# Optimization experiments

Measured on AMD Instinct MI355X. Metric: run time of the kernel, lower is better.

## Reference

```python
import jax, jax.numpy as jnp
import numpy as np

ALPHA_F, ALPHA_L, ALPHA_E, V_E = 0.1, 1.0, 1.0, 10.0
DF = float(np.exp(-ALPHA_F))
DL = float(np.exp(-ALPHA_L))
DE = float(np.exp(-ALPHA_E))

B, T, C, H, W = 8, 10, 32, 128, 128


def _fixed_weight(chans, dtype):
    # [[0.5,1,0.5],[1,0,1],[0.5,1,0.5]] broadcast to [C, C, 3, 3]
    k = jnp.array([[0.5, 1.0, 0.5], [1.0, 0.0, 1.0], [0.5, 1.0, 0.5]], dtype=dtype)
    return jnp.broadcast_to(k, (chans, chans, 3, 3))


def _conv(y, w):
    # 3x3 same-padding conv, NCHW / OIHW
    return jax.lax.conv_general_dilated(
        y, w, window_strides=(1, 1), padding='SAME',
        dimension_numbers=('NCHW', 'OIHW', 'NCHW'))


def setup_inputs() -> dict:
    key = jax.random.key(0)
    k1, k2, k3 = jax.random.split(key, 3)
    x = jax.random.normal(k1, (B, T, C, H, W), dtype=jnp.float32)
    # small-scale conv weights (fan-in-ish) to keep sigmoid in its dynamic range
    conv_w = jax.random.normal(k2, (C, C, 3, 3), dtype=jnp.float32) * 0.05
    conv_b = jax.random.normal(k3, (C,), dtype=jnp.float32) * 0.05
    return {'x': x, 'conv_w': conv_w, 'conv_b': conv_b}


def reference(x, conv_w, conv_b):
    b, t, c, h, w = x.shape
    wf = _fixed_weight(c, x.dtype)  # fixed, non-trainable feedback kernel
    bias = conv_b[None, :, None, None]

    def step(carry, x_t):
        f, l, e, y = carry
        f = DF * f + _conv(y, conv_w) + bias + x_t
        l = DL * l + _conv(y, wf)
        u = f + 0.5 * f * l
        e = DE * e + V_E * y
        y = jax.nn.sigmoid(u - e)
        return (f, l, e, y), y

    z = jnp.zeros((b, c, h, w), x.dtype)
    e0 = jnp.full((b, c, h, w), V_E / ALPHA_E, x.dtype)
    xs = jnp.moveaxis(x, 1, 0)  # [T, B, C, H, W]
    _, ys = jax.lax.scan(step, (z, z, e0, z), xs)
    return jnp.moveaxis(ys, 0, 1)  # [B, T, C, H, W]
```

## Files before the change

### kernel.cpp

```cpp
#include <hip/hip_runtime.h>
#include <math.h>

namespace {

constexpr int B = 8, T = 10, C = 32, H = 128, W = 128;
constexpr int HW = H * W;
constexpr int CHW = C * HW;
constexpr int BHW = B * HW;
constexpr long long NSTATE = (long long)B * CHW;

constexpr float DF = 0.90483741803595952f;
constexpr float DL = 0.36787944117144233f;
constexpr float DE = 0.36787944117144233f;
constexpr float VE = 10.0f;
constexpr float E0 = 3.6787944117144233f;

__global__ void k_wtr(const float* __restrict__ wgt, float* __restrict__ wtr) {
  int i = blockIdx.x * 256 + threadIdx.x;
  if (i >= C * C * 9) return;
  int ci = i / 288;
  int k = (i / 32) % 9;
  int co = i & 31;
  wtr[i] = wgt[co * 288 + ci * 9 + k];
}

__launch_bounds__(256, 2)
__global__ void k_step0(const float* __restrict__ x, const float* __restrict__ bias,
                        float* __restrict__ f, float* __restrict__ e,
                        float* __restrict__ lpl, float* __restrict__ out,
                        float* __restrict__ s_out) {
  __shared__ float sred[8][32][4];
  const int tid = threadIdx.x, bid = blockIdx.x;
  const int tw = bid & 7, th = (bid >> 3) & 15, b = bid >> 7;
  const int h0 = th * 8, w0 = tw * 16;
  const int g = tid >> 5, s = tid & 31;
  const int sh = s >> 2, sw = s & 3, cb = 4 * sw;
  const int gh = h0 + sh, gwc = w0 + cb;
  const float4 bc4 = *(const float4*)&bias[4 * g];
  const float bc[4] = {bc4.x, bc4.y, bc4.z, bc4.w};

  float sp[4] = {0.f, 0.f, 0.f, 0.f};
#pragma unroll
  for (int q = 0; q < 4; ++q) {
    const int c = 4 * g + q;
    const size_t sidx = (size_t)b * CHW + (size_t)c * HW + (size_t)gh * W + gwc;
    const size_t oidx = (((size_t)b * T) * C + c) * (size_t)HW + (size_t)gh * W + gwc;
    float4 x4 = *(const float4*)(x + oidx);
    float xr[4] = {x4.x, x4.y, x4.z, x4.w};
    float fo[4], eo[4], yn[4];
#pragma unroll
    for (int p = 0; p < 4; ++p) {
      float fn = bc[q] + xr[p];
      float yy = 1.f / (1.f + __expf(E0 - fn));
      fo[p] = fn;
      eo[p] = DE * E0 + VE * yy;
      yn[p] = yy;
      sp[p] += yy;
    }
    *(float4*)(f + sidx) = make_float4(fo[0], fo[1], fo[2], fo[3]);
    *(float4*)(e + sidx) = make_float4(eo[0], eo[1], eo[2], eo[3]);
    *(float4*)(out + oidx) = make_float4(yn[0], yn[1], yn[2], yn[3]);
  }
  *(float4*)&sred[g][s][0] = make_float4(sp[0], sp[1], sp[2], sp[3]);
  __syncthreads();
  if (tid < 32) {
    float4 a = *(const float4*)&sred[0][tid][0];
#pragma unroll
    for (int gg = 1; gg < 8; ++gg) {
      float4 bq = *(const float4*)&sred[gg][tid][0];
      a.x += bq.x; a.y += bq.y; a.z += bq.z; a.w += bq.w;
    }
    const size_t pidx = (size_t)b * HW + (size_t)gh * W + gwc;
    *(float4*)(s_out + pidx) = a;
    *(float4*)(lpl + pidx) = make_float4(0.f, 0.f, 0.f, 0.f);
  }
}

__launch_bounds__(256, 2)
__global__ void k_step(const float* __restrict__ x, const float* __restrict__ wtr,
                       const float* __restrict__ bias, const float* __restrict__ s_in,
                       float* __restrict__ s_out, float* __restrict__ f,
                       float* __restrict__ e, float* __restrict__ lpl,
                       float* __restrict__ out, int t) {
  __shared__ float ysl[8][10][28];
  __shared__ float wsl[8][9][32];
  __shared__ float sl[10][21];
  __shared__ float sred[8][32][4];

  const int tid = threadIdx.x, bid = blockIdx.x;
  const int tw = bid & 7, th = (bid >> 3) & 15, b = bid >> 7;
  const int h0 = th * 8, w0 = tw * 16;
  const int g = tid >> 5, s = tid & 31;
  const int sh = s >> 2, sw = s & 3, cb = 4 * sw;
  const int gh = h0 + sh, gwc = w0 + cb;

  const float* ybase = out + ((size_t)b * T + (t - 1)) * CHW;

  for (int i = tid; i < 180; i += 256) {
    int rr = i / 18, cl = i % 18;
    int gh2 = h0 - 1 + rr, gw2 = w0 - 1 + cl;
    float v = 0.f;
    if ((unsigned)gh2 < (unsigned)H && (unsigned)gw2 < (unsigned)W)
      v = s_in[(size_t)b * HW + gh2 * W + gw2];
    sl[rr][cl] = v;
  }

  float4 l4 = *(const float4*)(lpl + (size_t)b * HW + (size_t)gh * W + gwc);
  float lnew[4] = {l4.x, l4.y, l4.z, l4.w};

  const int i0 = tid;
  const int cil0 = i0 / 60, rr0 = (i0 % 60) / 6, j0 = i0 % 6;
  const int gh0p = h0 - 1 + rr0, ws0p = w0 - 4 + 4 * j0;
  const bool ok0 = (unsigned)gh0p < (unsigned)H && (unsigned)ws0p <= (unsigned)(W - 4);
  const size_t yoff0 = (size_t)cil0 * HW + (size_t)(ok0 ? gh0p * W + ws0p : 0);
  float* const yd0 = &ysl[cil0][rr0][4 * j0];
  const int i1 = tid + 256;
  const bool use1 = i1 < 480;
  const int cil1 = (i1 / 60) & 7, rr1 = (i1 % 60) / 6, j1 = i1 % 6;
  const int gh1p = h0 - 1 + rr1, ws1p = w0 - 4 + 4 * j1;
  const bool ok1 = use1 && (unsigned)gh1p < (unsigned)H &&
                   (unsigned)ws1p <= (unsigned)(W - 4);
  const size_t yoff1 = (size_t)cil1 * HW + (size_t)(ok1 ? gh1p * W + ws1p : 0);
  float* const yd1 = &ysl[cil1][rr1][4 * j1];

  const float4* const wsrc = (const float4*)wtr;
  float4* const wlds = (float4*)&wsl[0][0][0];

  float4 y0v, y1v, w0v, w1v, w2v;
  auto prefetch = [&](int cc) {
    const float* yb = ybase + (size_t)cc * 8 * HW;
    y0v = ok0 ? *(const float4*)(yb + yoff0) : make_float4(0.f, 0.f, 0.f, 0.f);
    y1v = ok1 ? *(const float4*)(yb + yoff1) : make_float4(0.f, 0.f, 0.f, 0.f);
    const float4* wb = wsrc + cc * 576;
    w0v = wb[tid];
    w1v = wb[tid + 256];
    w2v = (tid < 64) ? wb[tid + 512] : make_float4(0.f, 0.f, 0.f, 0.f);
  };
  prefetch(0);

  float acc[4][4] = {};

#pragma unroll 1
  for (int cc = 0; cc < 4; ++cc) {
    __syncthreads();
    yd0[0] = y0v.x; yd0[1] = y0v.y; yd0[2] = y0v.z; yd0[3] = y0v.w;
    if (use1) { yd1[0] = y1v.x; yd1[1] = y1v.y; yd1[2] = y1v.z; yd1[3] = y1v.w; }
    wlds[tid] = w0v;
    wlds[tid + 256] = w1v;
    if (tid < 64) wlds[tid + 512] = w2v;
    __syncthreads();
    if (cc < 3) prefetch(cc + 1);
    if (cc == 0) {
      float linc[4];
#pragma unroll
      for (int p = 0; p < 4; ++p) {
        const int c0 = cb + p;
        linc[p] = 0.5f * (sl[sh][c0] + sl[sh][c0 + 2] + sl[sh + 2][c0] +
                          sl[sh + 2][c0 + 2]) +
                  sl[sh][c0 + 1] + sl[sh + 2][c0 + 1] + sl[sh + 1][c0] +
                  sl[sh + 1][c0 + 2];
      }
#pragma unroll
      for (int p = 0; p < 4; ++p) lnew[p] = DL * lnew[p] + linc[p];
    }
#pragma unroll
    for (int cil = 0; cil < 8; ++cil) {
#pragma unroll
      for (int kh = 0; kh < 3; ++kh) {
        const float* rowp = &ysl[cil][sh + kh][0];
        float2 a2 = *(const float2*)(rowp + cb + 2);
        float4 m4 = *(const float4*)(rowp + cb + 4);
        float2 z2 = *(const float2*)(rowp + cb + 8);
        const float yrow[6] = {a2.y, m4.x, m4.y, m4.z, m4.w, z2.x};
#pragma unroll
        for (int kw = 0; kw < 3; ++kw) {
          float4 wk = *(const float4*)&wsl[cil][3 * kh + kw][4 * g];
          const float wq[4] = {wk.x, wk.y, wk.z, wk.w};
#pragma unroll
          for (int q = 0; q < 4; ++q)
#pragma unroll
            for (int p = 0; p < 4; ++p)
              acc[q][p] = fmaf(wq[q], yrow[p + kw], acc[q][p]);
        }
      }
    }
  }

  const float4 bc4 = *(const float4*)&bias[4 * g];
  const float bc[4] = {bc4.x, bc4.y, bc4.z, bc4.w};
  float sp[4] = {0.f, 0.f, 0.f, 0.f};
#pragma unroll
  for (int q = 0; q < 4; ++q) {
    const int c = 4 * g + q;
    const size_t sidx = (size_t)b * CHW + (size_t)c * HW + (size_t)gh * W + gwc;
    const size_t oidx = (((size_t)b * T + t) * C + c) * (size_t)HW + (size_t)gh * W + gwc;
    float4 f4 = *(const float4*)(f + sidx);
    float4 e4 = *(const float4*)(e + sidx);
    float4 x4 = *(const float4*)(x + oidx);
    float fr[4] = {f4.x, f4.y, f4.z, f4.w};
    float er[4] = {e4.x, e4.y, e4.z, e4.w};
    float xr[4] = {x4.x, x4.y, x4.z, x4.w};
    float fo[4], eo[4], yn[4];
#pragma unroll
    for (int p = 0; p < 4; ++p) {
      float fn = DF * fr[p] + acc[q][p] + bc[q] + xr[p];
      float u = fmaf(0.5f * fn, lnew[p], fn);
      float yy = 1.f / (1.f + __expf(er[p] - u));
      fo[p] = fn;
      eo[p] = DE * er[p] + VE * yy;
      yn[p] = yy;
      sp[p] += yy;
    }
    *(float4*)(f + sidx) = make_float4(fo[0], fo[1], fo[2], fo[3]);
    *(float4*)(e + sidx) = make_float4(eo[0], eo[1], eo[2], eo[3]);
    *(float4*)(out + oidx) = make_float4(yn[0], yn[1], yn[2], yn[3]);
  }
  *(float4*)&sred[g][s][0] = make_float4(sp[0], sp[1], sp[2], sp[3]);
  __syncthreads();
  if (tid < 32) {
    float4 a = *(const float4*)&sred[0][tid][0];
#pragma unroll
    for (int gg = 1; gg < 8; ++gg) {
      float4 bq = *(const float4*)&sred[gg][tid][0];
      a.x += bq.x; a.y += bq.y; a.z += bq.z; a.w += bq.w;
    }
    const size_t pidx = (size_t)b * HW + (size_t)gh * W + gwc;
    *(float4*)(s_out + pidx) = a;
    *(float4*)(lpl + pidx) = make_float4(lnew[0], lnew[1], lnew[2], lnew[3]);
  }
}

}

extern "C" void kernel_launch(void* const* d_in, const int* in_sizes, int n_in,
                              void* d_out, int out_size, void* d_ws, size_t ws_size,
                              hipStream_t stream) {
  (void)in_sizes; (void)n_in; (void)out_size; (void)ws_size;
  const float* x = (const float*)d_in[0];
  const float* wgt = (const float*)d_in[1];
  const float* bias = (const float*)d_in[2];
  float* out = (float*)d_out;

  float* ws = (float*)d_ws;
  float* f = ws;
  float* e = f + NSTATE;
  float* lpl = e + NSTATE;
  float* sA = lpl + BHW;
  float* sB = sA + BHW;
  float* wtr = sB + BHW;

  k_wtr<<<36, 256, 0, stream>>>(wgt, wtr);
  k_step0<<<1024, 256, 0, stream>>>(x, bias, f, e, lpl, out, sA);

  float* s_in = sA;
  float* s_out = sB;
  for (int t = 1; t < T; ++t) {
    k_step<<<1024, 256, 0, stream>>>(x, wtr, bias, s_in, s_out, f, e, lpl, out, t);
    float* tmp = s_in; s_in = s_out; s_out = tmp;
  }
}
```

Baseline: 609.5 us.

## Split output channels across two blocks per tile to double grid parallelism

Each spatial tile is now handled by two blocks, each computing 16 of the 32 output channels, which doubles the grid to 2048 blocks. Each half writes its own partial channel-sum plane, and the next step adds the two planes when building the fixed-kernel feedback. Only half 0 updates the lateral state. The goal is better occupancy and latency hiding with fewer accumulators per thread. The cost is that every block still loads the full 32-channel input halo, so global and LDS traffic for y roughly doubles.

```diff
diff --git a/kernel.cpp b/kernel.cpp
--- a/kernel.cpp
+++ b/kernel.cpp
@@ -72,6 +72,7 @@
     }
     const size_t pidx = (size_t)b * HW + (size_t)gh * W + gwc;
     *(float4*)(s_out + pidx) = a;
+    *(float4*)(s_out + BHW + pidx) = make_float4(0.f, 0.f, 0.f, 0.f);
     *(float4*)(lpl + pidx) = make_float4(0.f, 0.f, 0.f, 0.f);
   }
 }
@@ -83,16 +84,18 @@
                        float* __restrict__ e, float* __restrict__ lpl,
                        float* __restrict__ out, int t) {
   __shared__ float ysl[8][10][28];
-  __shared__ float wsl[8][9][32];
+  __shared__ float wsl[8][9][16];
   __shared__ float sl[10][21];
   __shared__ float sred[8][32][4];
 
   const int tid = threadIdx.x, bid = blockIdx.x;
-  const int tw = bid & 7, th = (bid >> 3) & 15, b = bid >> 7;
+  const int half = bid & 1;
+  const int tw = (bid >> 1) & 7, th = (bid >> 4) & 15, b = bid >> 8;
   const int h0 = th * 8, w0 = tw * 16;
   const int g = tid >> 5, s = tid & 31;
   const int sh = s >> 2, sw = s & 3, cb = 4 * sw;
   const int gh = h0 + sh, gwc = w0 + cb;
+  const int cob = 16 * half;
 
   const float* ybase = out + ((size_t)b * T + (t - 1)) * CHW;
 
@@ -100,8 +103,10 @@
     int rr = i / 18, cl = i % 18;
     int gh2 = h0 - 1 + rr, gw2 = w0 - 1 + cl;
     float v = 0.f;
-    if ((unsigned)gh2 < (unsigned)H && (unsigned)gw2 < (unsigned)W)
-      v = s_in[(size_t)b * HW + gh2 * W + gw2];
+    if ((unsigned)gh2 < (unsigned)H && (unsigned)gw2 < (unsigned)W) {
+      const size_t ii = (size_t)b * HW + gh2 * W + gw2;
+      v = s_in[ii] + s_in[BHW + ii];
+    }
     sl[rr][cl] = v;
   }
 
@@ -125,29 +130,31 @@
 
   const float4* const wsrc = (const float4*)wtr;
   float4* const wlds = (float4*)&wsl[0][0][0];
-
-  float4 y0v, y1v, w0v, w1v, w2v;
+  const int wsl0 = tid;
+  const int wc0 = wsl0 / 36, wk0 = (wsl0 % 36) / 4, wj0 = wsl0 & 3;
+  const int wslot1 = tid + 256;
+  const bool wuse1 = wslot1 < 288;
+  const int wc1 = (wslot1 / 36) & 7, wk1 = (wslot1 % 36) / 4, wj1 = wslot1 & 3;
+
+  float4 y0v, y1v, w0v, w1v;
   auto prefetch = [&](int cc) {
     const float* yb = ybase + (size_t)cc * 8 * HW;
     y0v = ok0 ? *(const float4*)(yb + yoff0) : make_float4(0.f, 0.f, 0.f, 0.f);
     y1v = ok1 ? *(const float4*)(yb + yoff1) : make_float4(0.f, 0.f, 0.f, 0.f);
-    const float4* wb = wsrc + cc * 576;
-    w0v = wb[tid];
-    w1v = wb[tid + 256];
-    w2v = (tid < 64) ? wb[tid + 512] : make_float4(0.f, 0.f, 0.f, 0.f);
+    w0v = wsrc[((cc * 8 + wc0) * 9 + wk0) * 8 + 4 * half + wj0];
+    if (wuse1) w1v = wsrc[((cc * 8 + wc1) * 9 + wk1) * 8 + 4 * half + wj1];
   };
   prefetch(0);
 
-  float acc[4][4] = {};
+  float acc[2][4] = {};
 
 #pragma unroll 1
   for (int cc = 0; cc < 4; ++cc) {
     __syncthreads();
     yd0[0] = y0v.x; yd0[1] = y0v.y; yd0[2] = y0v.z; yd0[3] = y0v.w;
     if (use1) { yd1[0] = y1v.x; yd1[1] = y1v.y; yd1[2] = y1v.z; yd1[3] = y1v.w; }
-    wlds[tid] = w0v;
-    wlds[tid + 256] = w1v;
-    if (tid < 64) wlds[tid + 512] = w2v;
+    wlds[wsl0] = w0v;
+    if (wuse1) wlds[wslot1] = w1v;
     __syncthreads();
     if (cc < 3) prefetch(cc + 1);
     if (cc == 0) {
@@ -174,10 +181,10 @@
         const float yrow[6] = {a2.y, m4.x, m4.y, m4.z, m4.w, z2.x};
 #pragma unroll
         for (int kw = 0; kw < 3; ++kw) {
-          float4 wk = *(const float4*)&wsl[cil][3 * kh + kw][4 * g];
-          const float wq[4] = {wk.x, wk.y, wk.z, wk.w};
-#pragma unroll
-          for (int q = 0; q < 4; ++q)
+          float2 wk = *(const float2*)&wsl[cil][3 * kh + kw][2 * g];
+          const float wq[2] = {wk.x, wk.y};
+#pragma unroll
+          for (int q = 0; q < 2; ++q)
 #pragma unroll
             for (int p = 0; p < 4; ++p)
               acc[q][p] = fmaf(wq[q], yrow[p + kw], acc[q][p]);
@@ -186,12 +193,12 @@
     }
   }
 
-  const float4 bc4 = *(const float4*)&bias[4 * g];
-  const float bc[4] = {bc4.x, bc4.y, bc4.z, bc4.w};
+  const float2 bc2 = *(const float2*)&bias[cob + 2 * g];
+  const float bc[2] = {bc2.x, bc2.y};
   float sp[4] = {0.f, 0.f, 0.f, 0.f};
 #pragma unroll
-  for (int q = 0; q < 4; ++q) {
-    const int c = 4 * g + q;
+  for (int q = 0; q < 2; ++q) {
+    const int c = cob + 2 * g + q;
     const size_t sidx = (size_t)b * CHW + (size_t)c * HW + (size_t)gh * W + gwc;
     const size_t oidx = (((size_t)b * T + t) * C + c) * (size_t)HW + (size_t)gh * W + gwc;
     float4 f4 = *(const float4*)(f + sidx);
@@ -225,8 +232,9 @@
       a.x += bq.x; a.y += bq.y; a.z += bq.z; a.w += bq.w;
     }
     const size_t pidx = (size_t)b * HW + (size_t)gh * W + gwc;
-    *(float4*)(s_out + pidx) = a;
-    *(float4*)(lpl + pidx) = make_float4(lnew[0], lnew[1], lnew[2], lnew[3]);
+    *(float4*)(s_out + (size_t)half * BHW + pidx) = a;
+    if (half == 0)
+      *(float4*)(lpl + pidx) = make_float4(lnew[0], lnew[1], lnew[2], lnew[3]);
   }
 }
 
@@ -246,8 +254,8 @@
   float* e = f + NSTATE;
   float* lpl = e + NSTATE;
   float* sA = lpl + BHW;
-  float* sB = sA + BHW;
-  float* wtr = sB + BHW;
+  float* sB = sA + 2 * BHW;
+  float* wtr = sB + 2 * BHW;
 
   k_wtr<<<36, 256, 0, stream>>>(wgt, wtr);
   k_step0<<<1024, 256, 0, stream>>>(x, bias, f, e, lpl, out, sA);
@@ -255,7 +263,7 @@
   float* s_in = sA;
   float* s_out = sB;
   for (int t = 1; t < T; ++t) {
-    k_step<<<1024, 256, 0, stream>>>(x, wtr, bias, s_in, s_out, f, e, lpl, out, t);
+    k_step<<<2048, 256, 0, stream>>>(x, wtr, bias, s_in, s_out, f, e, lpl, out, t);
     float* tmp = s_in; s_in = s_out; s_out = tmp;
   }
 }
```

New measurement: 967.6 us. 1.59x slower.

## Remap block IDs across XCDs and prefetch f/e state during last conv chunk

Applied to the files above, without the earlier changes.

Block indices are permuted so consecutive hardware block IDs, which are dispatched round-robin across XCDs, map to spatially contiguous tiles. Each XCD then works on one batch slice and its halo reads hit a shared L2. The conv loop is restructured so the last channel chunk is peeled off, and the f and e state loads are issued before that chunk's FMAs to hide their global latency. This costs 32 extra live registers per thread for the prefetched state, which could hurt occupancy at launch bounds of 2 blocks.

```diff
diff --git a/kernel.cpp b/kernel.cpp
--- a/kernel.cpp
+++ b/kernel.cpp
@@ -31,7 +31,8 @@
                         float* __restrict__ s_out) {
   __shared__ float sred[8][32][4];
   const int tid = threadIdx.x, bid = blockIdx.x;
-  const int tw = bid & 7, th = (bid >> 3) & 15, b = bid >> 7;
+  const int wg = (bid & 7) * 128 + (bid >> 3);
+  const int tw = wg & 7, th = (wg >> 3) & 15, b = wg >> 7;
   const int h0 = th * 8, w0 = tw * 16;
   const int g = tid >> 5, s = tid & 31;
   const int sh = s >> 2, sw = s & 3, cb = 4 * sw;
@@ -88,7 +89,8 @@
   __shared__ float sred[8][32][4];
 
   const int tid = threadIdx.x, bid = blockIdx.x;
-  const int tw = bid & 7, th = (bid >> 3) & 15, b = bid >> 7;
+  const int wg = (bid & 7) * 128 + (bid >> 3);
+  const int tw = wg & 7, th = (wg >> 3) & 15, b = wg >> 7;
   const int h0 = th * 8, w0 = tw * 16;
   const int g = tid >> 5, s = tid & 31;
   const int sh = s >> 2, sw = s & 3, cb = 4 * sw;
@@ -136,20 +138,47 @@
     w1v = wb[tid + 256];
     w2v = (tid < 64) ? wb[tid + 512] : make_float4(0.f, 0.f, 0.f, 0.f);
   };
-  prefetch(0);
-
-  float acc[4][4] = {};
-
-#pragma unroll 1
-  for (int cc = 0; cc < 4; ++cc) {
-    __syncthreads();
+  auto commit = [&]() {
     yd0[0] = y0v.x; yd0[1] = y0v.y; yd0[2] = y0v.z; yd0[3] = y0v.w;
     if (use1) { yd1[0] = y1v.x; yd1[1] = y1v.y; yd1[2] = y1v.z; yd1[3] = y1v.w; }
     wlds[tid] = w0v;
     wlds[tid + 256] = w1v;
     if (tid < 64) wlds[tid + 512] = w2v;
+  };
+  prefetch(0);
+
+  float acc[4][4] = {};
+
+  auto conv_chunk = [&]() {
+#pragma unroll
+    for (int cil = 0; cil < 8; ++cil) {
+#pragma unroll
+      for (int kh = 0; kh < 3; ++kh) {
+        const float* rowp = &ysl[cil][sh + kh][0];
+        float2 a2 = *(const float2*)(rowp + cb + 2);
+        float4 m4 = *(const float4*)(rowp + cb + 4);
+        float2 z2 = *(const float2*)(rowp + cb + 8);
+        const float yrow[6] = {a2.y, m4.x, m4.y, m4.z, m4.w, z2.x};
+#pragma unroll
+        for (int kw = 0; kw < 3; ++kw) {
+          float4 wk = *(const float4*)&wsl[cil][3 * kh + kw][4 * g];
+          const float wq[4] = {wk.x, wk.y, wk.z, wk.w};
+#pragma unroll
+          for (int q = 0; q < 4; ++q)
+#pragma unroll
+            for (int p = 0; p < 4; ++p)
+              acc[q][p] = fmaf(wq[q], yrow[p + kw], acc[q][p]);
+        }
+      }
+    }
+  };
+
+#pragma unroll 1
+  for (int cc = 0; cc < 3; ++cc) {
     __syncthreads();
-    if (cc < 3) prefetch(cc + 1);
+    commit();
+    __syncthreads();
+    prefetch(cc + 1);
     if (cc == 0) {
       float linc[4];
 #pragma unroll
@@ -163,28 +192,21 @@
 #pragma unroll
       for (int p = 0; p < 4; ++p) lnew[p] = DL * lnew[p] + linc[p];
     }
-#pragma unroll
-    for (int cil = 0; cil < 8; ++cil) {
-#pragma unroll
-      for (int kh = 0; kh < 3; ++kh) {
-        const float* rowp = &ysl[cil][sh + kh][0];
-        float2 a2 = *(const float2*)(rowp + cb + 2);
-        float4 m4 = *(const float4*)(rowp + cb + 4);
-        float2 z2 = *(const float2*)(rowp + cb + 8);
-        const float yrow[6] = {a2.y, m4.x, m4.y, m4.z, m4.w, z2.x};
-#pragma unroll
-        for (int kw = 0; kw < 3; ++kw) {
-          float4 wk = *(const float4*)&wsl[cil][3 * kh + kw][4 * g];
-          const float wq[4] = {wk.x, wk.y, wk.z, wk.w};
-#pragma unroll
-          for (int q = 0; q < 4; ++q)
-#pragma unroll
-            for (int p = 0; p < 4; ++p)
-              acc[q][p] = fmaf(wq[q], yrow[p + kw], acc[q][p]);
-        }
-      }
-    }
-  }
+    conv_chunk();
+  }
+
+  __syncthreads();
+  commit();
+  __syncthreads();
+  float4 fq4[4], eq4[4];
+#pragma unroll
+  for (int q = 0; q < 4; ++q) {
+    const size_t sidx =
+        (size_t)b * CHW + (size_t)(4 * g + q) * HW + (size_t)gh * W + gwc;
+    fq4[q] = *(const float4*)(f + sidx);
+    eq4[q] = *(const float4*)(e + sidx);
+  }
+  conv_chunk();
 
   const float4 bc4 = *(const float4*)&bias[4 * g];
   const float bc[4] = {bc4.x, bc4.y, bc4.z, bc4.w};
@@ -194,11 +216,9 @@
     const int c = 4 * g + q;
     const size_t sidx = (size_t)b * CHW + (size_t)c * HW + (size_t)gh * W + gwc;
     const size_t oidx = (((size_t)b * T + t) * C + c) * (size_t)HW + (size_t)gh * W + gwc;
-    float4 f4 = *(const float4*)(f + sidx);
-    float4 e4 = *(const float4*)(e + sidx);
     float4 x4 = *(const float4*)(x + oidx);
-    float fr[4] = {f4.x, f4.y, f4.z, f4.w};
-    float er[4] = {e4.x, e4.y, e4.z, e4.w};
+    float fr[4] = {fq4[q].x, fq4[q].y, fq4[q].z, fq4[q].w};
+    float er[4] = {eq4[q].x, eq4[q].y, eq4[q].z, eq4[q].w};
     float xr[4] = {x4.x, x4.y, x4.z, x4.w};
     float fo[4], eo[4], yn[4];
 #pragma unroll
```

Measured after the change: 569.9 us (median of 2 runs). 6.5% less time.
